# Optimization experiments

Hardware: AMD Instinct MI355X
Metric: run time of the kernel (lower is better)

Reference implementation:

```python
import jax, jax.numpy as jnp
import numpy as np

DIM = 1024
N_HEADS = 16
HEAD_DIM = DIM // N_HEADS
B, T = 2, 2048


def get_rotary_embedding(T, head_dim, dtype=jnp.float32):
    inv_freq = 1.0 / (10000.0 ** (jnp.arange(0, head_dim, 2, dtype=jnp.float32) / head_dim))
    t = jnp.arange(T, dtype=jnp.float32)
    freqs = jnp.einsum('t,f->tf', t, inv_freq)          # [T, head_dim/2]
    emb = jnp.concatenate([freqs, freqs], axis=-1)       # [T, head_dim]
    return jnp.sin(emb).astype(dtype), jnp.cos(emb).astype(dtype)


def rotate_half(x):
    x1, x2 = jnp.split(x, 2, axis=-1)
    return jnp.concatenate([-x2, x1], axis=-1)


def apply_rotary_pos_emb(x, sin, cos):
    # x: [B, H, T, D]; sin/cos: [T, D] broadcast over B, H
    return x * cos + rotate_half(x) * sin


def setup_inputs() -> dict:
    key = jax.random.key(0)
    ks = jax.random.split(key, 4)
    s = DIM ** -0.5
    return {
        'x': jax.random.normal(ks[0], (B, T, DIM), jnp.float32),
        'W_qkv': jax.random.normal(ks[1], (DIM, 3 * DIM), jnp.float32) * s,
        'b_qkv': jnp.zeros((3 * DIM,), jnp.float32),
        'W_out': jax.random.normal(ks[2], (DIM, DIM), jnp.float32) * s,
        'b_out': jnp.zeros((DIM,), jnp.float32),
    }


def reference(x, W_qkv, b_qkv, W_out, b_out):
    Bc, Tc, C = x.shape
    scale = HEAD_DIM ** -0.5
    qkv = x @ W_qkv + b_qkv                                    # [B, T, 3C]
    qkv = qkv.reshape(Bc, Tc, 3, N_HEADS, HEAD_DIM)
    qkv = jnp.transpose(qkv, (2, 0, 3, 1, 4))                  # [3, B, H, T, D]
    q, k, v = qkv[0], qkv[1], qkv[2]
    sin, cos = get_rotary_embedding(Tc, HEAD_DIM, x.dtype)
    q = apply_rotary_pos_emb(q, sin, cos)
    k = apply_rotary_pos_emb(k, sin, cos)
    attn = jnp.einsum('bhqd,bhkd->bhqk', q, k) * scale         # [B, H, T, T]
    probs = jax.nn.softmax(attn, axis=-1)
    out = jnp.einsum('bhqk,bhkd->bhqd', probs, v)              # [B, H, T, D]
    out = jnp.transpose(out, (0, 2, 1, 3)).reshape(Bc, Tc, C)
    return out @ W_out + b_out
```

## Files before the change

### kernel.cpp

```cpp
#include <hip/hip_runtime.h>
#include <hip/hip_bf16.h>
#include <cstdint>
#include <cstddef>

typedef unsigned short ushort_t;
typedef __bf16 bf16x8 __attribute__((ext_vector_type(8)));
typedef float f32x4 __attribute__((ext_vector_type(4)));

#define DEV static __device__ __forceinline__

DEV void gl2lds16(const void* g, void* l) {
  __builtin_amdgcn_global_load_lds(
      (const __attribute__((address_space(1))) void*)(uintptr_t)g,
      (__attribute__((address_space(3))) void*)(uintptr_t)l, 16, 0, 0);
}

DEV bf16x8 ldfrag(const void* p) { return __builtin_bit_cast(bf16x8, *(const uint4*)p); }

DEV bf16x8 ldb64pair(const void* p) {
  uint2 lo = *(const uint2*)p;
  uint2 hi = *(const uint2*)((const char*)p + 8);
  union { unsigned int u[4]; bf16x8 v; } x;
  x.u[0] = lo.x; x.u[1] = lo.y; x.u[2] = hi.x; x.u[3] = hi.y;
  return x.v;
}

DEV f32x4 mfma16(bf16x8 a, bf16x8 b, f32x4 c) {
  return __builtin_amdgcn_mfma_f32_16x16x32_bf16(a, b, c, 0, 0, 0);
}

DEV ushort_t f2b(float f) { return __builtin_bit_cast(ushort_t, __float2bfloat16(f)); }
DEV unsigned int cvtpk(float lo, float hi) {
  unsigned int r;
  asm("v_cvt_pk_bf16_f32 %0, %1, %2" : "=v"(r) : "v"(lo), "v"(hi));
  return r;
}
#if __has_builtin(__builtin_amdgcn_exp2f)
DEV float e2(float x) { return __builtin_amdgcn_exp2f(x); }
#else
DEV float e2(float x) { return exp2f(x); }
#endif

__global__ __launch_bounds__(256) void k_prep(const float* __restrict__ x,
                                              const float* __restrict__ Wqkv,
                                              const float* __restrict__ Wout,
                                              ushort_t* __restrict__ X16,
                                              ushort_t* __restrict__ WQT,
                                              ushort_t* __restrict__ WOT,
                                              float* __restrict__ sintab,
                                              float* __restrict__ costab) {
  __shared__ ushort_t tile[64][72];
  const int b = blockIdx.x, t = threadIdx.x;
  if (b < 4096) {
    int i = (b * 256 + t) * 4;
    float4 v = *(const float4*)(x + i);
    ushort4 o;
    o.x = f2b(v.x); o.y = f2b(v.y); o.z = f2b(v.z); o.w = f2b(v.w);
    *(ushort4*)(X16 + i) = o;
    return;
  }
  if (b < 5120) {
    const float* W; ushort_t* WT; int N, bb, Nb;
    if (b < 4864) { W = Wqkv; WT = WQT; N = 3072; bb = b - 4096; Nb = 48; }
    else          { W = Wout; WT = WOT; N = 1024; bb = b - 4864; Nb = 16; }
    const int n0 = (bb % Nb) * 64, k0 = (bb / Nb) * 64, K = 1024;
#pragma unroll
    for (int i = 0; i < 16; ++i) {
      int e = i * 256 + t; int r = e >> 6, c = e & 63;
      tile[c][r] = f2b(W[(size_t)(k0 + r) * N + n0 + c]);
    }
    __syncthreads();
#pragma unroll
    for (int i = 0; i < 16; ++i) {
      int e = i * 256 + t; int rn = e >> 6, ck = e & 63;
      WT[(size_t)(n0 + rn) * K + k0 + ck] = tile[rn][ck];
    }
    return;
  }
  int id = (b - 5120) * 256 + t;
  int f = id & 31, tt = id >> 5;
  float invf = e2(-(float)f * 0.4152410118609203f);
  float ang = (float)tt * invf;
  sintab[id] = sinf(ang);
  costab[id] = cosf(ang);
}

template <int EPI, int BM, int BN>
__global__ __launch_bounds__(256, 3) void k_gemm_bt(
    const ushort_t* __restrict__ A, const ushort_t* __restrict__ BT,
    const float* __restrict__ bias, ushort_t* __restrict__ Oq,
    ushort_t* __restrict__ Ok, ushort_t* __restrict__ Ov,
    float* __restrict__ Of, const float* __restrict__ sintab,
    const float* __restrict__ costab, int K, int N) {
  constexpr int MI = BM / 32, NJ = BN / 32;
  __shared__ __align__(16) char As[2][BM * 64];
  __shared__ __align__(16) char Bs[2][BN * 64];
  const int tid = threadIdx.x, lane = tid & 63, wv = tid >> 6;
  const int l15 = lane & 15, l4 = lane >> 4;
  const int nt = blockIdx.x, mt = blockIdx.y;
  const char* Ab = (const char*)(A + (size_t)mt * BM * K);
  const char* Bb = (const char*)(BT + (size_t)nt * BN * K);
  const int rs = K * 2;
  const int wr = (wv >> 1) * (BM / 2), wc = (wv & 1) * (BN / 2);
  f32x4 acc[MI][NJ] = {};
#pragma unroll
  for (int ii = 0; ii < BM / 64; ++ii) {
    int slot = wv * (BM / 64) + ii;
    int r = slot * 16 + (lane >> 2);
    int scb = ((lane & 3) * 16) ^ ((r & 3) << 4);
    gl2lds16(Ab + (size_t)r * rs + scb, As[0] + slot * 1024);
  }
#pragma unroll
  for (int ii = 0; ii < BN / 64; ++ii) {
    int slot = wv * (BN / 64) + ii;
    int r = slot * 16 + (lane >> 2);
    int scb = ((lane & 3) * 16) ^ ((r & 3) << 4);
    gl2lds16(Bb + (size_t)r * rs + scb, Bs[0] + slot * 1024);
  }
  __syncthreads();
  for (int k0 = 0; k0 < K; k0 += 32) {
    const int cur = (k0 >> 5) & 1;
    if (k0 + 32 < K) {
#pragma unroll
      for (int ii = 0; ii < BM / 64; ++ii) {
        int slot = wv * (BM / 64) + ii;
        int r = slot * 16 + (lane >> 2);
        int scb = ((lane & 3) * 16) ^ ((r & 3) << 4);
        gl2lds16(Ab + (size_t)r * rs + (k0 + 32) * 2 + scb, As[cur ^ 1] + slot * 1024);
      }
#pragma unroll
      for (int ii = 0; ii < BN / 64; ++ii) {
        int slot = wv * (BN / 64) + ii;
        int r = slot * 16 + (lane >> 2);
        int scb = ((lane & 3) * 16) ^ ((r & 3) << 4);
        gl2lds16(Bb + (size_t)r * rs + (k0 + 32) * 2 + scb, Bs[cur ^ 1] + slot * 1024);
      }
    }
    bf16x8 af[MI], bg[NJ];
#pragma unroll
    for (int i = 0; i < MI; ++i) {
      int r = wr + i * 16 + l15;
      af[i] = ldfrag(As[cur] + r * 64 + ((l4 * 16) ^ ((r & 3) << 4)));
    }
#pragma unroll
    for (int j = 0; j < NJ; ++j) {
      int r = wc + j * 16 + l15;
      bg[j] = ldfrag(Bs[cur] + r * 64 + ((l4 * 16) ^ ((r & 3) << 4)));
    }
    __builtin_amdgcn_s_setprio(1);
#pragma unroll
    for (int i = 0; i < MI; ++i)
#pragma unroll
      for (int j = 0; j < NJ; ++j)
        acc[i][j] = mfma16(af[i], bg[j], acc[i][j]);
    __builtin_amdgcn_s_setprio(0);
    __syncthreads();
  }
  if constexpr (EPI == 0) {
    const int colbase = nt * BN + wc;
    const int part = colbase >> 10;
    const int h = (colbase >> 6) & 15;
    float bv[NJ];
#pragma unroll
    for (int j = 0; j < NJ; ++j) bv[j] = bias[colbase + j * 16 + l15];
    if (part <= 1) {
      ushort_t* dst = part ? Ok : Oq;
      const float sc = part ? 1.0f : 0.18033688011112042f;
#pragma unroll
      for (int i = 0; i < MI; ++i) {
        int m0 = mt * BM + wr + i * 16 + l4 * 4;
#pragma unroll
        for (int e = 0; e < 4; ++e) {
          int row = m0 + e;
          int bb = row >> 11, t = row & 2047;
          size_t rb = ((size_t)(bb * 16 + h) * 2048 + t) * 64;
#pragma unroll
          for (int j = 0; j < 2; ++j) {
            int f = j * 16 + l15;
            float x1 = acc[i][j][e] + bv[j];
            float x2 = acc[i][j + 2][e] + bv[j + 2];
            float sn = sintab[t * 32 + f], cs = costab[t * 32 + f];
            dst[rb + f]      = f2b((x1 * cs - x2 * sn) * sc);
            dst[rb + f + 32] = f2b((x2 * cs + x1 * sn) * sc);
          }
        }
      }
    } else {
#pragma unroll
      for (int i = 0; i < MI; ++i) {
        int m0 = mt * BM + wr + i * 16 + l4 * 4;
        int bb = m0 >> 11, t0 = m0 & 2047;
#pragma unroll
        for (int j = 0; j < NJ; ++j) {
          int d = j * 16 + l15;
          ushort4 pk;
          pk.x = f2b(acc[i][j][0] + bv[j]);
          pk.y = f2b(acc[i][j][1] + bv[j]);
          pk.z = f2b(acc[i][j][2] + bv[j]);
          pk.w = f2b(acc[i][j][3] + bv[j]);
          *(ushort4*)(Ov + ((size_t)(bb * 16 + h) * 64 + d) * 2048 + t0) = pk;
        }
      }
    }
  } else {
#pragma unroll
    for (int j = 0; j < NJ; ++j) {
      int c = nt * BN + wc + j * 16 + l15;
      float bvv = bias[c];
#pragma unroll
      for (int i = 0; i < MI; ++i) {
        int m0 = mt * BM + wr + i * 16 + l4 * 4;
#pragma unroll
        for (int e = 0; e < 4; ++e)
          Of[(size_t)(m0 + e) * N + c] = acc[i][j][e] + bvv;
      }
    }
  }
}

__global__ __launch_bounds__(256, 3) void k_attn(const ushort_t* __restrict__ Q,
                                                 const ushort_t* __restrict__ K,
                                                 const ushort_t* __restrict__ VT,
                                                 ushort_t* __restrict__ AO) {
  __shared__ __align__(16) char Kt[2][8192];
  __shared__ __align__(16) char Vt[2][8192];
  __shared__ __align__(16) char Pl[4][4352];
  const int tid = threadIdx.x, lane = tid & 63, wv = tid >> 6;
  const int l15 = lane & 15, l4 = lane >> 4;
  const int lin = blockIdx.x + (blockIdx.y << 4);
  const int nl = ((lin & 7) << 6) + (lin >> 3);
  const int qt = nl & 15, bh = nl >> 4;
  const int qbase = qt * 128 + wv * 32;

  const char* Qb = (const char*)(Q + ((size_t)bh * 2048 + qbase) * 64);
  bf16x8 bq[2][2];
#pragma unroll
  for (int qh = 0; qh < 2; ++qh)
#pragma unroll
    for (int c = 0; c < 2; ++c)
      bq[qh][c] = ldfrag(Qb + (qh * 16 + l15) * 128 + c * 64 + l4 * 16);

  const char* Kbase = (const char*)(K + (size_t)bh * 2048 * 64);
  const char* Vbase = (const char*)(VT + (size_t)bh * 64 * 2048);
  char* Pw = Pl[wv];

  const int sr = lane >> 3;
  const int scb = ((lane & 7) * 16) ^ ((sr & 7) << 4);

  const f32x4 mInit = {-16.f, -16.f, -16.f, -16.f};
  const uint4 onebits = {0x3F803F80u, 0x3F803F80u, 0x3F803F80u, 0x3F803F80u};
  const bf16x8 vones = __builtin_bit_cast(bf16x8, onebits);
  f32x4 oden[2] = {};
  f32x4 o[2][4] = {};

#pragma unroll
  for (int ii = 0; ii < 2; ++ii) {
    int slot = wv * 2 + ii;
    int r = slot * 8 + sr;
    gl2lds16(Kbase + (size_t)r * 128 + scb, Kt[0] + slot * 1024);
    gl2lds16(Vbase + (size_t)r * 4096 + scb, Vt[0] + slot * 1024);
  }
  __syncthreads();

  for (int kt = 0; kt < 32; ++kt) {
    const int cur = kt & 1;
    if (kt < 31) {
#pragma unroll
      for (int ii = 0; ii < 2; ++ii) {
        int slot = wv * 2 + ii;
        int r = slot * 8 + sr;
        gl2lds16(Kbase + ((size_t)((kt + 1) * 64 + r)) * 128 + scb, Kt[cur ^ 1] + slot * 1024);
        gl2lds16(Vbase + (size_t)r * 4096 + (kt + 1) * 128 + scb, Vt[cur ^ 1] + slot * 1024);
      }
    }
    const char* Kb = Kt[cur];
    const char* Vb = Vt[cur];
    const int sw = (l15 & 7) << 4;

    f32x4 s[2][4];
    __builtin_amdgcn_s_setprio(1);
#pragma unroll
    for (int j = 0; j < 4; ++j) {
      int r = j * 16 + l15;
      bf16x8 k0 = ldfrag(Kb + r * 128 + ((l4 * 16) ^ sw));
      bf16x8 k1 = ldfrag(Kb + r * 128 + ((64 + l4 * 16) ^ sw));
#pragma unroll
      for (int qh = 0; qh < 2; ++qh) {
        f32x4 z = mfma16(k0, bq[qh][0], mInit);
        s[qh][j] = mfma16(k1, bq[qh][1], z);
      }
    }
    __builtin_amdgcn_s_setprio(0);

#pragma unroll
    for (int qh = 0; qh < 2; ++qh) {
#pragma unroll
      for (int j = 0; j < 4; ++j) {
        uint2 w;
        w.x = cvtpk(e2(s[qh][j][0]), e2(s[qh][j][1]));
        w.y = cvtpk(e2(s[qh][j][2]), e2(s[qh][j][3]));
        *(uint2*)(Pw + (qh * 16 + l15) * 136 + j * 32 + l4 * 8) = w;
      }
    }

    __builtin_amdgcn_s_setprio(1);
#pragma unroll
    for (int c = 0; c < 2; ++c) {
      bf16x8 bp[2];
#pragma unroll
      for (int qh = 0; qh < 2; ++qh)
        bp[qh] = ldb64pair(Pw + (qh * 16 + l15) * 136 + c * 64 + l4 * 16);
#pragma unroll
      for (int qh = 0; qh < 2; ++qh)
        oden[qh] = mfma16(vones, bp[qh], oden[qh]);
#pragma unroll
      for (int dt = 0; dt < 4; ++dt) {
        int r = dt * 16 + l15;
        bf16x8 av = ldfrag(Vb + r * 128 + ((c * 64 + l4 * 16) ^ sw));
#pragma unroll
        for (int qh = 0; qh < 2; ++qh) o[qh][dt] = mfma16(av, bp[qh], o[qh][dt]);
      }
    }
    __builtin_amdgcn_s_setprio(0);
    __syncthreads();
  }

  const int b = bh >> 4, h = bh & 15;
#pragma unroll
  for (int qh = 0; qh < 2; ++qh) {
    float inv = 1.0f / oden[qh][0];
    int q = qbase + qh * 16 + l15;
    ushort_t* dst = AO + ((size_t)(b * 2048 + q)) * 1024 + h * 64;
#pragma unroll
    for (int dt = 0; dt < 4; ++dt) {
      ushort4 pk;
      pk.x = f2b(o[qh][dt][0] * inv);
      pk.y = f2b(o[qh][dt][1] * inv);
      pk.z = f2b(o[qh][dt][2] * inv);
      pk.w = f2b(o[qh][dt][3] * inv);
      *(ushort4*)(dst + dt * 16 + l4 * 4) = pk;
    }
  }
}

extern "C" void kernel_launch(void* const* d_in, const int* in_sizes, int n_in,
                              void* d_out, int out_size, void* d_ws, size_t ws_size,
                              hipStream_t stream) {
  (void)in_sizes; (void)n_in; (void)out_size;
  const float* x    = (const float*)d_in[0];
  const float* Wqkv = (const float*)d_in[1];
  const float* bqkv = (const float*)d_in[2];
  const float* Wout = (const float*)d_in[3];
  const float* bout = (const float*)d_in[4];
  float* out = (float*)d_out;
  char* ws = (char*)d_ws;

  ushort_t* X16 = (ushort_t*)(ws + 0);
  ushort_t* WQT = (ushort_t*)(ws + 8388608);
  ushort_t* WOT = (ushort_t*)(ws + 14680064);
  ushort_t* QB  = (ushort_t*)(ws + 16777216);
  ushort_t* KB  = (ushort_t*)(ws + 25165824);
  ushort_t* VTT = (ushort_t*)(ws + 33554432);
  float* SINT   = (float*)(ws + 41943040);
  float* COST   = SINT + 65536;
  ushort_t* AO  = X16;

  if (ws_size < (size_t)42467328) return;

  k_prep<<<5376, 256, 0, stream>>>(x, Wqkv, Wout, X16, WQT, WOT, SINT, COST);
  k_gemm_bt<0, 128, 128><<<dim3(24, 32), 256, 0, stream>>>(
      X16, WQT, bqkv, QB, KB, VTT, nullptr, SINT, COST, 1024, 3072);
  k_attn<<<dim3(16, 32), 256, 0, stream>>>(QB, KB, VTT, AO);
  k_gemm_bt<1, 64, 128><<<dim3(8, 64), 256, 0, stream>>>(
      AO, WOT, bout, nullptr, nullptr, nullptr, out, nullptr, nullptr, 1024, 1024);
}
```

Before: 107.9 us.

## Triple-buffer K/V tiles in attention with prefetch two tiles ahead

Moves the attention kernel's K/V LDS staging from double to triple buffering, issuing loads for tile kt+2 while tile kt is computed. Explicit vmcnt waits and a single barrier per iteration replace the trailing __syncthreads. The goal is to hide global-to-LDS latency better and cut synchronization. LDS use grows by 16KB per block, which may lower occupancy from the 3 blocks per CU requested in launch bounds.

```diff
diff --git a/kernel.cpp b/kernel.cpp
--- a/kernel.cpp
+++ b/kernel.cpp
@@ -222,8 +222,8 @@
                                                  const ushort_t* __restrict__ K,
                                                  const ushort_t* __restrict__ VT,
                                                  ushort_t* __restrict__ AO) {
-  __shared__ __align__(16) char Kt[2][8192];
-  __shared__ __align__(16) char Vt[2][8192];
+  __shared__ __align__(16) char Kt[3][8192];
+  __shared__ __align__(16) char Vt[3][8192];
   __shared__ __align__(16) char Pl[4][4352];
   const int tid = threadIdx.x, lane = tid & 63, wv = tid >> 6;
   const int l15 = lane & 15, l4 = lane >> 4;
@@ -246,36 +246,38 @@
 
   const int sr = lane >> 3;
   const int scb = ((lane & 7) * 16) ^ ((sr & 7) << 4);
+  const int slot0 = wv * 2, slot1 = wv * 2 + 1;
+  const int r0 = slot0 * 8 + sr, r1 = slot1 * 8 + sr;
 
   const f32x4 mInit = {-16.f, -16.f, -16.f, -16.f};
   const uint4 onebits = {0x3F803F80u, 0x3F803F80u, 0x3F803F80u, 0x3F803F80u};
   const bf16x8 vones = __builtin_bit_cast(bf16x8, onebits);
   f32x4 oden[2] = {};
   f32x4 o[2][4] = {};
-
-#pragma unroll
-  for (int ii = 0; ii < 2; ++ii) {
-    int slot = wv * 2 + ii;
-    int r = slot * 8 + sr;
-    gl2lds16(Kbase + (size_t)r * 128 + scb, Kt[0] + slot * 1024);
-    gl2lds16(Vbase + (size_t)r * 4096 + scb, Vt[0] + slot * 1024);
-  }
-  __syncthreads();
-
+  const int sw = (l15 & 7) << 4;
+
+#define STAGE_KV(t, buf)                                                          \
+  do {                                                                            \
+    gl2lds16(Kbase + ((size_t)((t) * 64 + r0)) * 128 + scb, Kt[buf] + slot0 * 1024); \
+    gl2lds16(Kbase + ((size_t)((t) * 64 + r1)) * 128 + scb, Kt[buf] + slot1 * 1024); \
+    gl2lds16(Vbase + (size_t)r0 * 4096 + (t) * 128 + scb, Vt[buf] + slot0 * 1024);   \
+    gl2lds16(Vbase + (size_t)r1 * 4096 + (t) * 128 + scb, Vt[buf] + slot1 * 1024);   \
+  } while (0)
+
+  STAGE_KV(0, 0);
+  STAGE_KV(1, 1);
+
+  int cur = 0, s2 = 2;
   for (int kt = 0; kt < 32; ++kt) {
-    const int cur = kt & 1;
-    if (kt < 31) {
-#pragma unroll
-      for (int ii = 0; ii < 2; ++ii) {
-        int slot = wv * 2 + ii;
-        int r = slot * 8 + sr;
-        gl2lds16(Kbase + ((size_t)((kt + 1) * 64 + r)) * 128 + scb, Kt[cur ^ 1] + slot * 1024);
-        gl2lds16(Vbase + (size_t)r * 4096 + (kt + 1) * 128 + scb, Vt[cur ^ 1] + slot * 1024);
-      }
-    }
+    if (kt < 31) asm volatile("s_waitcnt vmcnt(4)" ::: "memory");
+    else         asm volatile("s_waitcnt vmcnt(0)" ::: "memory");
+    __builtin_amdgcn_s_barrier();
+    __builtin_amdgcn_sched_barrier(0);
+    if (kt + 2 < 32) STAGE_KV(kt + 2, s2);
+    __builtin_amdgcn_sched_barrier(0);
+
     const char* Kb = Kt[cur];
     const char* Vb = Vt[cur];
-    const int sw = (l15 & 7) << 4;
 
     f32x4 s[2][4];
     __builtin_amdgcn_s_setprio(1);
@@ -322,8 +324,11 @@
       }
     }
     __builtin_amdgcn_s_setprio(0);
-    __syncthreads();
-  }
+
+    cur = cur + 1 < 3 ? cur + 1 : 0;
+    s2 = s2 + 1 < 3 ? s2 + 1 : 0;
+  }
+#undef STAGE_KV
 
   const int b = bh >> 4, h = bh & 15;
 #pragma unroll
```

After: 114.1 us. 5.7% more time.

## Halve attention query tile per block to double grid size

Applied to the files above, without the earlier changes.

Each wave now handles 16 query rows instead of 32, so a block covers 64 queries and the attention grid grows from 512 to 1024 blocks, with the block-to-(head, q-tile) swizzle adjusted to match. The aim is more parallelism and less register/LDS pressure (the P buffer is halved) so more waves fit per CU. In exchange, each K/V tile loaded into LDS is reused by half as many queries, doubling total K/V global traffic and LDS fill work per unit of compute.

```diff
diff --git a/kernel.cpp b/kernel.cpp
--- a/kernel.cpp
+++ b/kernel.cpp
@@ -224,21 +224,19 @@
                                                  ushort_t* __restrict__ AO) {
   __shared__ __align__(16) char Kt[2][8192];
   __shared__ __align__(16) char Vt[2][8192];
-  __shared__ __align__(16) char Pl[4][4352];
+  __shared__ __align__(16) char Pl[4][2176];
   const int tid = threadIdx.x, lane = tid & 63, wv = tid >> 6;
   const int l15 = lane & 15, l4 = lane >> 4;
-  const int lin = blockIdx.x + (blockIdx.y << 4);
-  const int nl = ((lin & 7) << 6) + (lin >> 3);
-  const int qt = nl & 15, bh = nl >> 4;
-  const int qbase = qt * 128 + wv * 32;
+  const int lin = blockIdx.x;
+  const int nl = ((lin & 7) << 7) | (lin >> 3);
+  const int qt = nl & 31, bh = nl >> 5;
+  const int qbase = qt * 64 + wv * 16;
 
   const char* Qb = (const char*)(Q + ((size_t)bh * 2048 + qbase) * 64);
-  bf16x8 bq[2][2];
-#pragma unroll
-  for (int qh = 0; qh < 2; ++qh)
-#pragma unroll
-    for (int c = 0; c < 2; ++c)
-      bq[qh][c] = ldfrag(Qb + (qh * 16 + l15) * 128 + c * 64 + l4 * 16);
+  bf16x8 bq[2];
+#pragma unroll
+  for (int c = 0; c < 2; ++c)
+    bq[c] = ldfrag(Qb + l15 * 128 + c * 64 + l4 * 16);
 
   const char* Kbase = (const char*)(K + (size_t)bh * 2048 * 64);
   const char* Vbase = (const char*)(VT + (size_t)bh * 64 * 2048);
@@ -250,8 +248,8 @@
   const f32x4 mInit = {-16.f, -16.f, -16.f, -16.f};
   const uint4 onebits = {0x3F803F80u, 0x3F803F80u, 0x3F803F80u, 0x3F803F80u};
   const bf16x8 vones = __builtin_bit_cast(bf16x8, onebits);
-  f32x4 oden[2] = {};
-  f32x4 o[2][4] = {};
+  f32x4 oden = {};
+  f32x4 o[4] = {};
 
 #pragma unroll
   for (int ii = 0; ii < 2; ++ii) {
@@ -277,48 +275,36 @@
     const char* Vb = Vt[cur];
     const int sw = (l15 & 7) << 4;
 
-    f32x4 s[2][4];
+    f32x4 s[4];
     __builtin_amdgcn_s_setprio(1);
 #pragma unroll
     for (int j = 0; j < 4; ++j) {
       int r = j * 16 + l15;
       bf16x8 k0 = ldfrag(Kb + r * 128 + ((l4 * 16) ^ sw));
       bf16x8 k1 = ldfrag(Kb + r * 128 + ((64 + l4 * 16) ^ sw));
-#pragma unroll
-      for (int qh = 0; qh < 2; ++qh) {
-        f32x4 z = mfma16(k0, bq[qh][0], mInit);
-        s[qh][j] = mfma16(k1, bq[qh][1], z);
-      }
+      f32x4 z = mfma16(k0, bq[0], mInit);
+      s[j] = mfma16(k1, bq[1], z);
     }
     __builtin_amdgcn_s_setprio(0);
 
 #pragma unroll
-    for (int qh = 0; qh < 2; ++qh) {
-#pragma unroll
-      for (int j = 0; j < 4; ++j) {
-        uint2 w;
-        w.x = cvtpk(e2(s[qh][j][0]), e2(s[qh][j][1]));
-        w.y = cvtpk(e2(s[qh][j][2]), e2(s[qh][j][3]));
-        *(uint2*)(Pw + (qh * 16 + l15) * 136 + j * 32 + l4 * 8) = w;
-      }
+    for (int j = 0; j < 4; ++j) {
+      uint2 w;
+      w.x = cvtpk(e2(s[j][0]), e2(s[j][1]));
+      w.y = cvtpk(e2(s[j][2]), e2(s[j][3]));
+      *(uint2*)(Pw + l15 * 136 + j * 32 + l4 * 8) = w;
     }
 
     __builtin_amdgcn_s_setprio(1);
 #pragma unroll
     for (int c = 0; c < 2; ++c) {
-      bf16x8 bp[2];
-#pragma unroll
-      for (int qh = 0; qh < 2; ++qh)
-        bp[qh] = ldb64pair(Pw + (qh * 16 + l15) * 136 + c * 64 + l4 * 16);
-#pragma unroll
-      for (int qh = 0; qh < 2; ++qh)
-        oden[qh] = mfma16(vones, bp[qh], oden[qh]);
+      bf16x8 bp = ldb64pair(Pw + l15 * 136 + c * 64 + l4 * 16);
+      oden = mfma16(vones, bp, oden);
 #pragma unroll
       for (int dt = 0; dt < 4; ++dt) {
         int r = dt * 16 + l15;
         bf16x8 av = ldfrag(Vb + r * 128 + ((c * 64 + l4 * 16) ^ sw));
-#pragma unroll
-        for (int qh = 0; qh < 2; ++qh) o[qh][dt] = mfma16(av, bp[qh], o[qh][dt]);
+        o[dt] = mfma16(av, bp, o[dt]);
       }
     }
     __builtin_amdgcn_s_setprio(0);
@@ -326,20 +312,17 @@
   }
 
   const int b = bh >> 4, h = bh & 15;
-#pragma unroll
-  for (int qh = 0; qh < 2; ++qh) {
-    float inv = 1.0f / oden[qh][0];
-    int q = qbase + qh * 16 + l15;
-    ushort_t* dst = AO + ((size_t)(b * 2048 + q)) * 1024 + h * 64;
-#pragma unroll
-    for (int dt = 0; dt < 4; ++dt) {
-      ushort4 pk;
-      pk.x = f2b(o[qh][dt][0] * inv);
-      pk.y = f2b(o[qh][dt][1] * inv);
-      pk.z = f2b(o[qh][dt][2] * inv);
-      pk.w = f2b(o[qh][dt][3] * inv);
-      *(ushort4*)(dst + dt * 16 + l4 * 4) = pk;
-    }
+  float inv = 1.0f / oden[0];
+  int q = qbase + l15;
+  ushort_t* dst = AO + ((size_t)(b * 2048 + q)) * 1024 + h * 64;
+#pragma unroll
+  for (int dt = 0; dt < 4; ++dt) {
+    ushort4 pk;
+    pk.x = f2b(o[dt][0] * inv);
+    pk.y = f2b(o[dt][1] * inv);
+    pk.z = f2b(o[dt][2] * inv);
+    pk.w = f2b(o[dt][3] * inv);
+    *(ushort4*)(dst + dt * 16 + l4 * 4) = pk;
   }
 }
 
@@ -370,7 +353,7 @@
   k_prep<<<5376, 256, 0, stream>>>(x, Wqkv, Wout, X16, WQT, WOT, SINT, COST);
   k_gemm_bt<0, 128, 128><<<dim3(24, 32), 256, 0, stream>>>(
       X16, WQT, bqkv, QB, KB, VTT, nullptr, SINT, COST, 1024, 3072);
-  k_attn<<<dim3(16, 32), 256, 0, stream>>>(QB, KB, VTT, AO);
+  k_attn<<<1024, 256, 0, stream>>>(QB, KB, VTT, AO);
   k_gemm_bt<1, 64, 128><<<dim3(8, 64), 256, 0, stream>>>(
       AO, WOT, bout, nullptr, nullptr, nullptr, out, nullptr, nullptr, 1024, 1024);
 }
```

Result: slower. 119.0 us (+10.2%).
